# Performance work log

Measured on AMD Instinct MI355X. Metric: run time of the kernel, lower is better.

## Reference

```python
import jax, jax.numpy as jnp
import numpy as np

B, IN, D1, H1, H2, NC = 16384, 1024, 8, 2048, 1024, 1000
C = IN // D1  # 128 channels, D=8 each
EPS = 1e-5


def _bn(x, g, b):
    # training-mode BatchNorm1d: biased variance over batch dim
    m = jnp.mean(x, axis=0)
    v = jnp.var(x, axis=0)
    return (x - m) * jax.lax.rsqrt(v + EPS) * g + b


def setup_inputs() -> dict:
    key = jax.random.key(0)
    ks = jax.random.split(key, 18)
    f = jax.random.normal
    return {
        "x": f(ks[0], (B, IN), jnp.float32),
        "norm0_g": 1.0 + 0.1 * f(ks[1], (IN,), jnp.float32),
        "norm0_b": 0.1 * f(ks[2], (IN,), jnp.float32),
        "S": f(ks[3], (C, D1, 15), jnp.float32),
        "Hm": f(ks[4], (15, 16), jnp.float32),
        "T": f(ks[5], (C, 15), jnp.float32),
        "LUT": f(ks[6], (C, 16, D1), jnp.float32),
        "W1": 0.02 * f(ks[7], (H1, IN), jnp.float32),
        "b1": 0.02 * f(ks[8], (H1,), jnp.float32),
        "norm1_g": 1.0 + 0.1 * f(ks[9], (H1,), jnp.float32),
        "norm1_b": 0.1 * f(ks[10], (H1,), jnp.float32),
        "W2": 0.02 * f(ks[11], (H2, H1), jnp.float32),
        "b2": 0.02 * f(ks[12], (H2,), jnp.float32),
        "norm2_g": 1.0 + 0.1 * f(ks[13], (H2,), jnp.float32),
        "norm2_b": 0.1 * f(ks[14], (H2,), jnp.float32),
        "W3": 0.02 * f(ks[15], (NC, H2), jnp.float32),
        "b3": 0.02 * f(ks[16], (NC,), jnp.float32),
    }


def reference(x, norm0_g, norm0_b, S, Hm, T, LUT, W1, b1,
              norm1_g, norm1_b, W2, b2, norm2_g, norm2_b, W3, b3):
    h = _bn(x, norm0_g, norm0_b)
    # --- MM block: per-channel small GEMMs + STE sign + STE argmax LUT ---
    xc = h.reshape(-1, C, D1)                          # [B, C, D]
    z = jnp.einsum('bcd,cdk->bck', xc, S) - T - 1e-4   # [B, C, 15]
    t = jnp.tanh(z)
    q = jax.lax.stop_gradient(jnp.sign(z) - t) + t     # STE sign
    logits = jnp.einsum('bck,kj->bcj', q, Hm)          # [B, C, 16]
    one_hot = jax.nn.one_hot(jnp.argmax(logits, axis=-1), 16, dtype=logits.dtype)
    sm = jax.nn.softmax(logits, axis=-1)
    oh_out = jnp.einsum('bck,ckd->bcd', one_hot, LUT)
    sm_out = jnp.einsum('bck,ckd->bcd', sm, LUT)
    v = jax.lax.stop_gradient(oh_out - sm_out) + sm_out  # STE argmax select
    v = v.reshape(-1, C * D1)                           # [B, IN]
    # --- MLP head ---
    h1 = jax.nn.relu(_bn(v @ W1.T + b1, norm1_g, norm1_b))
    h2 = jax.nn.relu(_bn(h1 @ W2.T + b2, norm2_g, norm2_b))
    logits3 = h2 @ W3.T + b3
    return jax.nn.log_softmax(logits3, axis=-1), h1
```

## Files before the change

kernel.cpp:

```cpp
#include <hip/hip_runtime.h>

typedef unsigned short u16;
typedef __attribute__((ext_vector_type(8))) short bf16x8;
typedef __attribute__((ext_vector_type(4))) float f32x4;
typedef __attribute__((ext_vector_type(4))) u16 u16x4;
typedef __attribute__((ext_vector_type(8))) u16 u16x8;

__device__ __forceinline__ u16 f2bf(float f) {
    union { float f; unsigned u; } v; v.f = f;
    unsigned u = v.u;
    unsigned r = (u + 0x7fffu + ((u >> 16) & 1u)) >> 16;
    return (u16)r;
}
__device__ __forceinline__ float bf2f(u16 u) {
    union { unsigned u; float f; } v; v.u = ((unsigned)u) << 16;
    return v.f;
}

__device__ __forceinline__ void gload16(const u16* g, u16* l) {
    __builtin_amdgcn_global_load_lds((const __attribute__((address_space(1))) void*)g,
                                     (__attribute__((address_space(3))) void*)l, 16, 0, 0);
}

#define WAITV(N) asm volatile("s_waitcnt vmcnt(" #N ")" ::: "memory")

__device__ __forceinline__ void sbar() {
    __builtin_amdgcn_sched_barrier(0);
    __builtin_amdgcn_s_barrier();
    __builtin_amdgcn_sched_barrier(0);
}

__device__ __forceinline__ void cvt4(const float* in, u16* out, int i) {
    f32x4 v = *(const f32x4*)(in + (size_t)i * 4);
    u16x4 o;
    o.x = f2bf(v.x); o.y = f2bf(v.y); o.z = f2bf(v.z); o.w = f2bf(v.w);
    *(u16x4*)(out + (size_t)i * 4) = o;
}

__global__ __launch_bounds__(256) void leaf_kernel(
    const float* __restrict__ W1, const float* __restrict__ W2, const float* __restrict__ W3,
    u16* __restrict__ W1b, u16* __restrict__ W2b, u16* __restrict__ W3b,
    const float* __restrict__ x, float* __restrict__ part0) {
    int bid = blockIdx.x;
    if (bid < 5120) {
        int i = bid * 256 + threadIdx.x;
        if (i < 524288) {
            cvt4(W1, W1b, i);
        } else if (i < 1048576) {
            cvt4(W2, W2b, i - 524288);
        } else {
            int j = i - 1048576;
            int e = j * 4;
            int row = e >> 10;
            u16x4 o;
            if (row < 1000) {
                f32x4 v = *(const f32x4*)(W3 + e);
                o.x = f2bf(v.x); o.y = f2bf(v.y); o.z = f2bf(v.z); o.w = f2bf(v.w);
            } else {
                o.x = 0; o.y = 0; o.z = 0; o.w = 0;
            }
            *(u16x4*)(W3b + e) = o;
        }
    } else {
        int by = bid - 5120;
        int col = threadIdx.x * 4;
        long base = (long)by * 32 * 1024 + col;
        f32x4 s = {0.f, 0.f, 0.f, 0.f};
        f32x4 q = {0.f, 0.f, 0.f, 0.f};
        for (int r = 0; r < 32; ++r) {
            f32x4 v = *(const f32x4*)(x + base + (long)r * 1024);
            s.x += v.x; s.y += v.y; s.z += v.z; s.w += v.w;
            q.x = fmaf(v.x, v.x, q.x); q.y = fmaf(v.y, v.y, q.y);
            q.z = fmaf(v.z, v.z, q.z); q.w = fmaf(v.w, v.w, q.w);
        }
        long o = ((long)by * 1024 + col) * 2;
        f32x4 p0 = {s.x, q.x, s.y, q.y};
        f32x4 p1 = {s.z, q.z, s.w, q.w};
        *(f32x4*)(part0 + o) = p0;
        *(f32x4*)(part0 + o + 4) = p1;
    }
}

__global__ __launch_bounds__(256) void col_stats_finalize(
    const float* __restrict__ part, int cols, int nblk, float inv_n,
    const float* __restrict__ g, const float* __restrict__ b, float* __restrict__ ab) {
    __shared__ float red[8][64];
    int cl = threadIdx.x & 31;
    int j = threadIdx.x >> 5;
    int col = blockIdx.x * 32 + cl;
    int per = nblk / 8;
    float s = 0.f, ss = 0.f;
    for (int i = 0; i < per; ++i) {
        long o = ((long)(j * per + i) * cols + col) * 2;
        s += part[o]; ss += part[o + 1];
    }
    red[j][cl * 2] = s;
    red[j][cl * 2 + 1] = ss;
    __syncthreads();
    if (threadIdx.x < 32) {
        int c = blockIdx.x * 32 + threadIdx.x;
        float fs = 0.f, fss = 0.f;
#pragma unroll
        for (int jj = 0; jj < 8; ++jj) {
            fs += red[jj][threadIdx.x * 2];
            fss += red[jj][threadIdx.x * 2 + 1];
        }
        float m = fs * inv_n;
        float var = fss * inv_n - m * m;
        float a = g[c] * rsqrtf(var + 1e-5f);
        ab[c * 2 + 0] = a;
        ab[c * 2 + 1] = b[c] - m * a;
    }
}

__global__ __launch_bounds__(256) void mm_block_kernel(
    const float* __restrict__ x, const float* __restrict__ ab0,
    const float* __restrict__ S, const float* __restrict__ Tt,
    const float* __restrict__ Hm, const float* __restrict__ LUT,
    u16* __restrict__ v) {
    __shared__ float sS[480];
    __shared__ float sT[60];
    __shared__ float sHm[240];
    __shared__ float sLUT[512];
    __shared__ float sAB[64];
    const int t = threadIdx.x;
    const int cb = blockIdx.y * 4;

    for (int i = t; i < 480; i += 256) sS[i] = S[cb * 120 + i];
    for (int i = t; i < 60; i += 256)  sT[i] = Tt[cb * 15 + i];
    for (int i = t; i < 240; i += 256) sHm[i] = Hm[i];
    for (int i = t; i < 512; i += 256) sLUT[i] = LUT[cb * 128 + i];
    for (int i = t; i < 64; i += 256)  sAB[i] = ab0[cb * 16 + i];
    __syncthreads();

    const int row = blockIdx.x * 256 + t;
    const float* xp = x + (size_t)row * 1024 + cb * 8;
    float xr[32];
#pragma unroll
    for (int i = 0; i < 8; ++i) {
        f32x4 v4 = *(const f32x4*)(xp + i * 4);
        xr[i * 4 + 0] = v4.x; xr[i * 4 + 1] = v4.y;
        xr[i * 4 + 2] = v4.z; xr[i * 4 + 3] = v4.w;
    }
    u16 ov[32];
#pragma unroll
    for (int ch = 0; ch < 4; ++ch) {
        float h[8];
#pragma unroll
        for (int d = 0; d < 8; ++d)
            h[d] = xr[ch * 8 + d] * sAB[ch * 16 + d * 2] + sAB[ch * 16 + d * 2 + 1];
        float lg[16];
#pragma unroll
        for (int j = 0; j < 16; ++j) lg[j] = 0.f;
        for (int k = 0; k < 15; ++k) {
            float a = 0.f;
#pragma unroll
            for (int d = 0; d < 8; ++d) a = fmaf(h[d], sS[ch * 120 + d * 15 + k], a);
            float z = (a - sT[ch * 15 + k]) - 1e-4f;
            float q = (z > 0.f) ? 1.f : ((z < 0.f) ? -1.f : 0.f);
#pragma unroll
            for (int j = 0; j < 16; ++j) lg[j] = fmaf(q, sHm[k * 16 + j], lg[j]);
        }
        int jb = 0; float best = lg[0];
#pragma unroll
        for (int j = 1; j < 16; ++j) { if (lg[j] > best) { best = lg[j]; jb = j; } }
#pragma unroll
        for (int d = 0; d < 8; ++d) ov[ch * 8 + d] = f2bf(sLUT[ch * 128 + jb * 8 + d]);
    }
    u16* vp = v + (size_t)row * 1024 + cb * 8;
#pragma unroll
    for (int ch = 0; ch < 4; ++ch)
        *(u16x8*)(vp + ch * 8) = *(u16x8*)&ov[ch * 8];
}

__global__ __launch_bounds__(256) void bn_relu_apply8(
    const u16* __restrict__ y, const float* __restrict__ ab, int cols, int total8,
    float* __restrict__ out_f32, u16* __restrict__ out_b16) {
    int i = blockIdx.x * 256 + threadIdx.x;
    if (i >= total8) return;
    long e = (long)i * 8;
    int col = (int)(e % cols);
    u16x8 yv = *(const u16x8*)(y + e);
    float r[8];
#pragma unroll
    for (int d = 0; d < 8; ++d)
        r[d] = fmaxf(bf2f(yv[d]) * ab[(col + d) * 2] + ab[(col + d) * 2 + 1], 0.f);
    if (out_f32) {
        f32x4 rf0 = {r[0], r[1], r[2], r[3]};
        f32x4 rf1 = {r[4], r[5], r[6], r[7]};
        *(f32x4*)(out_f32 + e) = rf0;
        *(f32x4*)(out_f32 + e + 4) = rf1;
    }
    u16x8 o;
#pragma unroll
    for (int d = 0; d < 8; ++d) o[d] = f2bf(r[d]);
    *(u16x8*)(out_b16 + e) = o;
}

#define MFMA16(a, b, c) __builtin_amdgcn_mfma_f32_16x16x32_bf16(a, b, c, 0, 0, 0)

template <bool STORE_BF16, bool DO_STATS, bool WRITER>
__global__ __launch_bounds__(512, 2) void gemm256(
    const u16* __restrict__ A, const u16* __restrict__ Bm, void* __restrict__ Cv,
    const float* __restrict__ bias, float* __restrict__ part,
    int M, int N, int K, int ldc, int ncol,
    const u16* __restrict__ wsrc, float* __restrict__ wdst, long wn4) {
    extern __shared__ u16 lds[];
    const int t = threadIdx.x;
    const int gyG = WRITER ? ((int)gridDim.y - 2) : (int)gridDim.y;
    if (WRITER && (int)blockIdx.y >= gyG) {
        long wblk = (long)((int)blockIdx.y - gyG) * gridDim.x + blockIdx.x;
        long tid = wblk * 512 + t;
        for (long c = tid; c < wn4; c += 65536) {
            u16x4 v = *(const u16x4*)(wsrc + c * 4);
            f32x4 o = {bf2f(v.x), bf2f(v.y), bf2f(v.z), bf2f(v.w)};
            __builtin_nontemporal_store(o, (f32x4*)(wdst + c * 4));
        }
        return;
    }
    const int BOFF = 32768;
    const int lane = t & 63, w = t >> 6;
    const int wr = w >> 2, wc = w & 3;
    const int fr = lane & 15, kg = lane >> 4;
    const int gx = gridDim.x;
    const int nwg = gx * gyG;
    const int flat = blockIdx.y * gx + blockIdx.x;
    const int swz = (flat & 7) * (nwg >> 3) + (flat >> 3);
    const int bm = (swz % gx) * 256;
    const int bn = (swz / gx) * 256;
    const int NT = K >> 6;

    const int srow8 = lane >> 3;
    const int scc = (lane & 7) ^ srow8;
    const int L0 = w * 2;
    const u16* gAb = A + ((size_t)bm + L0 * 8 + srow8) * K + scc * 8;
    const u16* gBb = Bm + ((size_t)bn + L0 * 8 + srow8) * K + scc * 8;
    u16* ldsW = lds + L0 * 512 + lane * 8;

    const int s0 = (kg ^ (fr & 7)) * 8;
    const int s1 = s0 ^ 32;
    int rA[4], rB[2];
#pragma unroll
    for (int i = 0; i < 4; ++i) rA[i] = (i * 32 + wr * 16 + fr) * 64;
#pragma unroll
    for (int p = 0; p < 2; ++p) rB[p] = (p * 64 + wc * 16 + fr) * 64;

    f32x4 acc[8][4];
#pragma unroll
    for (int m = 0; m < 8; ++m)
#pragma unroll
        for (int n = 0; n < 4; ++n) acc[m][n] = (f32x4){0.f, 0.f, 0.f, 0.f};

    bf16x8 Ar[8][2], Br[2][2];

#define STG(gp, matOff, d, half, k0)                                          \
    {                                                                         \
        u16* dst_ = ldsW + (matOff) + ((d) * 2 + (half)) * 8192;              \
        const u16* src_ = (gp) + (size_t)((half) * 128) * K + (k0);           \
        gload16(src_, dst_);                                                  \
        gload16(src_ + (size_t)8 * K, dst_ + 512);                            \
    }
#define LDF(off) (*(const bf16x8*)&lds[off])

    STG(gAb, 0, 0, 0, 0);
    STG(gBb, BOFF, 0, 0, 0);
    STG(gAb, 0, 0, 1, 0);
    STG(gBb, BOFF, 0, 1, 0);

#pragma unroll 2
    for (int tt = 0; tt < NT - 1; ++tt) {
        const int d = tt & 1, dn = d ^ 1;
        const int k0n = (tt + 1) << 6;
        const int a0 = (d * 2) * 8192, a1 = (d * 2 + 1) * 8192;
        const int b0 = BOFF + a0, b1 = BOFF + a1;
        WAITV(4); sbar();
        STG(gAb, 0, dn, 0, k0n);
#pragma unroll
        for (int i = 0; i < 4; ++i) { Ar[i][0] = LDF(a0 + rA[i] + s0); Ar[i][1] = LDF(a0 + rA[i] + s1); }
#pragma unroll
        for (int p = 0; p < 2; ++p) { Br[p][0] = LDF(b0 + rB[p] + s0); Br[p][1] = LDF(b0 + rB[p] + s1); }
        __builtin_amdgcn_s_setprio(1);
#pragma unroll
        for (int i = 0; i < 4; ++i)
#pragma unroll
            for (int p = 0; p < 2; ++p) {
                acc[i][p] = MFMA16(Ar[i][0], Br[p][0], acc[i][p]);
                acc[i][p] = MFMA16(Ar[i][1], Br[p][1], acc[i][p]);
            }
        __builtin_amdgcn_s_setprio(0);
        WAITV(4); sbar();
        STG(gBb, BOFF, dn, 0, k0n);
#pragma unroll
        for (int i = 0; i < 4; ++i) { Ar[4 + i][0] = LDF(a1 + rA[i] + s0); Ar[4 + i][1] = LDF(a1 + rA[i] + s1); }
        __builtin_amdgcn_s_setprio(1);
#pragma unroll
        for (int i = 0; i < 4; ++i)
#pragma unroll
            for (int p = 0; p < 2; ++p) {
                acc[4 + i][p] = MFMA16(Ar[4 + i][0], Br[p][0], acc[4 + i][p]);
                acc[4 + i][p] = MFMA16(Ar[4 + i][1], Br[p][1], acc[4 + i][p]);
            }
        __builtin_amdgcn_s_setprio(0);
        WAITV(4); sbar();
        STG(gAb, 0, dn, 1, k0n);
#pragma unroll
        for (int p = 0; p < 2; ++p) { Br[p][0] = LDF(b1 + rB[p] + s0); Br[p][1] = LDF(b1 + rB[p] + s1); }
        __builtin_amdgcn_s_setprio(1);
#pragma unroll
        for (int i = 0; i < 4; ++i)
#pragma unroll
            for (int p = 0; p < 2; ++p) {
                acc[4 + i][2 + p] = MFMA16(Ar[4 + i][0], Br[p][0], acc[4 + i][2 + p]);
                acc[4 + i][2 + p] = MFMA16(Ar[4 + i][1], Br[p][1], acc[4 + i][2 + p]);
            }
        __builtin_amdgcn_s_setprio(0);
        STG(gBb, BOFF, dn, 1, k0n);
        __builtin_amdgcn_s_setprio(1);
#pragma unroll
        for (int i = 0; i < 4; ++i)
#pragma unroll
            for (int p = 0; p < 2; ++p) {
                acc[i][2 + p] = MFMA16(Ar[i][0], Br[p][0], acc[i][2 + p]);
                acc[i][2 + p] = MFMA16(Ar[i][1], Br[p][1], acc[i][2 + p]);
            }
        __builtin_amdgcn_s_setprio(0);
    }
    {
        const int d = (NT - 1) & 1;
        const int a0 = (d * 2) * 8192, a1 = (d * 2 + 1) * 8192;
        const int b0 = BOFF + a0, b1 = BOFF + a1;
        WAITV(4); sbar();
#pragma unroll
        for (int i = 0; i < 4; ++i) { Ar[i][0] = LDF(a0 + rA[i] + s0); Ar[i][1] = LDF(a0 + rA[i] + s1); }
#pragma unroll
        for (int p = 0; p < 2; ++p) { Br[p][0] = LDF(b0 + rB[p] + s0); Br[p][1] = LDF(b0 + rB[p] + s1); }
        __builtin_amdgcn_s_setprio(1);
#pragma unroll
        for (int i = 0; i < 4; ++i)
#pragma unroll
            for (int p = 0; p < 2; ++p) {
                acc[i][p] = MFMA16(Ar[i][0], Br[p][0], acc[i][p]);
                acc[i][p] = MFMA16(Ar[i][1], Br[p][1], acc[i][p]);
            }
        __builtin_amdgcn_s_setprio(0);
        WAITV(2); sbar();
#pragma unroll
        for (int i = 0; i < 4; ++i) { Ar[4 + i][0] = LDF(a1 + rA[i] + s0); Ar[4 + i][1] = LDF(a1 + rA[i] + s1); }
        __builtin_amdgcn_s_setprio(1);
#pragma unroll
        for (int i = 0; i < 4; ++i)
#pragma unroll
            for (int p = 0; p < 2; ++p) {
                acc[4 + i][p] = MFMA16(Ar[4 + i][0], Br[p][0], acc[4 + i][p]);
                acc[4 + i][p] = MFMA16(Ar[4 + i][1], Br[p][1], acc[4 + i][p]);
            }
        __builtin_amdgcn_s_setprio(0);
        WAITV(0); sbar();
#pragma unroll
        for (int p = 0; p < 2; ++p) { Br[p][0] = LDF(b1 + rB[p] + s0); Br[p][1] = LDF(b1 + rB[p] + s1); }
        __builtin_amdgcn_s_setprio(1);
#pragma unroll
        for (int i = 0; i < 4; ++i)
#pragma unroll
            for (int p = 0; p < 2; ++p) {
                acc[4 + i][2 + p] = MFMA16(Ar[4 + i][0], Br[p][0], acc[4 + i][2 + p]);
                acc[4 + i][2 + p] = MFMA16(Ar[4 + i][1], Br[p][1], acc[4 + i][2 + p]);
                acc[i][2 + p] = MFMA16(Ar[i][0], Br[p][0], acc[i][2 + p]);
                acc[i][2 + p] = MFMA16(Ar[i][1], Br[p][1], acc[i][2 + p]);
            }
        __builtin_amdgcn_s_setprio(0);
    }

    const int fq = lane >> 4;
    if (STORE_BF16) {
        u16* C = (u16*)Cv;
        u16* sm = lds;
        const int orow = t >> 4;
        const int ocol = (t & 15) * 16;
#pragma unroll
        for (int m = 0; m < 8; ++m) {
            __syncthreads();
#pragma unroll
            for (int n = 0; n < 4; ++n)
#pragma unroll
                for (int j = 0; j < 4; ++j)
                    sm[(wr * 16 + fq * 4 + j) * 256 + n * 64 + wc * 16 + fr] = f2bf(acc[m][n][j]);
            __syncthreads();
            u16x8 o0 = *(const u16x8*)&sm[orow * 256 + ocol];
            u16x8 o1 = *(const u16x8*)&sm[orow * 256 + ocol + 8];
            u16* cp = C + (size_t)(bm + m * 32 + orow) * ldc + bn + ocol;
            *(u16x8*)cp = o0;
            *(u16x8*)(cp + 8) = o1;
        }
    } else {
#pragma unroll
        for (int m = 0; m < 8; ++m) {
#pragma unroll
            for (int n = 0; n < 4; ++n) {
                int row = bm + m * 32 + wr * 16 + fq * 4;
                int col = bn + n * 64 + wc * 16 + fr;
                if (col < ncol) {
                    float* C = (float*)Cv;
                    float bv = bias ? bias[col] : 0.f;
#pragma unroll
                    for (int j = 0; j < 4; ++j)
                        C[(size_t)(row + j) * ldc + col] = acc[m][n][j] + bv;
                }
            }
        }
    }

    if (DO_STATS) {
        __syncthreads();
        float* smf = (float*)lds;
        float sv[4], qv[4];
#pragma unroll
        for (int n = 0; n < 4; ++n) {
            float s = 0.f, q = 0.f;
#pragma unroll
            for (int m = 0; m < 8; ++m)
#pragma unroll
                for (int j = 0; j < 4; ++j) {
                    float vv = acc[m][n][j];
                    s += vv;
                    q = fmaf(vv, vv, q);
                }
            s += __shfl_xor(s, 16); s += __shfl_xor(s, 32);
            q += __shfl_xor(q, 16); q += __shfl_xor(q, 32);
            sv[n] = s; qv[n] = q;
        }
        if (lane < 16) {
#pragma unroll
            for (int n = 0; n < 4; ++n) {
                smf[(w * 64 + n * 16 + lane) * 2 + 0] = sv[n];
                smf[(w * 64 + n * 16 + lane) * 2 + 1] = qv[n];
            }
        }
        __syncthreads();
        if (t < 256) {
            int n = t >> 6, wcq = (t >> 4) & 3, frq = t & 15;
            int i0 = (wcq * 64 + n * 16 + frq) * 2;
            int i1 = ((4 + wcq) * 64 + n * 16 + frq) * 2;
            long o = ((long)(bm >> 8) * N + bn + t) * 2;
            part[o] = smf[i0] + smf[i1];
            part[o + 1] = smf[i0 + 1] + smf[i1 + 1];
        }
    }
#undef STG
#undef LDF
}

__global__ __launch_bounds__(256) void log_softmax_wave(float* __restrict__ y) {
    const int w = threadIdx.x >> 6;
    const int lane = threadIdx.x & 63;
    float* p = y + ((size_t)blockIdx.x * 4 + w) * 1000;
    const bool has3 = lane < 58;
    f32x4 v0 = ((const f32x4*)p)[lane];
    f32x4 v1 = ((const f32x4*)p)[lane + 64];
    f32x4 v2 = ((const f32x4*)p)[lane + 128];
    f32x4 v3 = has3 ? ((const f32x4*)p)[lane + 192]
                    : (f32x4){-1e30f, -1e30f, -1e30f, -1e30f};
    float m = fmaxf(fmaxf(fmaxf(v0.x, v0.y), fmaxf(v0.z, v0.w)),
                    fmaxf(fmaxf(v1.x, v1.y), fmaxf(v1.z, v1.w)));
    m = fmaxf(m, fmaxf(fmaxf(v2.x, v2.y), fmaxf(v2.z, v2.w)));
    m = fmaxf(m, fmaxf(fmaxf(v3.x, v3.y), fmaxf(v3.z, v3.w)));
#pragma unroll
    for (int d = 32; d > 0; d >>= 1) m = fmaxf(m, __shfl_xor(m, d));
    float sum = expf(v0.x - m) + expf(v0.y - m) + expf(v0.z - m) + expf(v0.w - m)
              + expf(v1.x - m) + expf(v1.y - m) + expf(v1.z - m) + expf(v1.w - m)
              + expf(v2.x - m) + expf(v2.y - m) + expf(v2.z - m) + expf(v2.w - m)
              + expf(v3.x - m) + expf(v3.y - m) + expf(v3.z - m) + expf(v3.w - m);
#pragma unroll
    for (int d = 32; d > 0; d >>= 1) sum += __shfl_xor(sum, d);
    float lse = m + logf(sum);
    v0.x -= lse; v0.y -= lse; v0.z -= lse; v0.w -= lse;
    v1.x -= lse; v1.y -= lse; v1.z -= lse; v1.w -= lse;
    v2.x -= lse; v2.y -= lse; v2.z -= lse; v2.w -= lse;
    __builtin_nontemporal_store(v0, &((f32x4*)p)[lane]);
    __builtin_nontemporal_store(v1, &((f32x4*)p)[lane + 64]);
    __builtin_nontemporal_store(v2, &((f32x4*)p)[lane + 128]);
    if (has3) {
        v3.x -= lse; v3.y -= lse; v3.z -= lse; v3.w -= lse;
        __builtin_nontemporal_store(v3, &((f32x4*)p)[lane + 192]);
    }
}

extern "C" void kernel_launch(void* const* d_in, const int* in_sizes, int n_in,
                              void* d_out, int out_size, void* d_ws, size_t ws_size,
                              hipStream_t stream) {
    const float* x   = (const float*)d_in[0];
    const float* n0g = (const float*)d_in[1];
    const float* n0b = (const float*)d_in[2];
    const float* S   = (const float*)d_in[3];
    const float* Hm  = (const float*)d_in[4];
    const float* Tt  = (const float*)d_in[5];
    const float* LUT = (const float*)d_in[6];
    const float* W1  = (const float*)d_in[7];
    const float* n1g = (const float*)d_in[9];
    const float* n1b = (const float*)d_in[10];
    const float* W2  = (const float*)d_in[11];
    const float* n2g = (const float*)d_in[13];
    const float* n2b = (const float*)d_in[14];
    const float* W3  = (const float*)d_in[15];
    const float* b3  = (const float*)d_in[16];

    const int B = 16384, IN = 1024, H1 = 2048, H2 = 1024;
    const int NBY0 = 512;

    hipFuncSetAttribute((const void*)&gemm256<true, true, false>,
                        hipFuncAttributeMaxDynamicSharedMemorySize, 131072);
    hipFuncSetAttribute((const void*)&gemm256<true, true, true>,
                        hipFuncAttributeMaxDynamicSharedMemorySize, 131072);
    hipFuncSetAttribute((const void*)&gemm256<false, false, false>,
                        hipFuncAttributeMaxDynamicSharedMemorySize, 131072);

    char* ws = (char*)d_ws;
    size_t off = 0;
    auto alloc = [&](size_t bytes) -> char* {
        char* p = ws + off;
        off += (bytes + 255) & ~(size_t)255;
        return p;
    };
    float* ab0  = (float*)alloc(IN * 2 * sizeof(float));
    float* ab1  = (float*)alloc(H1 * 2 * sizeof(float));
    float* ab2  = (float*)alloc(H2 * 2 * sizeof(float));
    float* part0 = (float*)alloc((size_t)NBY0 * IN * 2 * sizeof(float));
    float* part1 = (float*)alloc((size_t)(B / 256) * H1 * 2 * sizeof(float));
    float* part2 = (float*)alloc((size_t)(B / 256) * H2 * 2 * sizeof(float));
    u16* W1b = (u16*)alloc((size_t)H1 * IN * 2);
    u16* W2b = (u16*)alloc((size_t)H2 * H1 * 2);
    u16* W3b = (u16*)alloc((size_t)1024 * 1024 * 2);
    u16* vb  = (u16*)alloc((size_t)B * IN * 2);
    u16* y1b = (u16*)alloc((size_t)B * H1 * 2);

    float* out0 = (float*)d_out;
    float* out1 = out0 + (size_t)B * 1000;

    leaf_kernel<<<5120 + NBY0, 256, 0, stream>>>(W1, W2, W3, W1b, W2b, W3b, x, part0);

    col_stats_finalize<<<IN / 32, 256, 0, stream>>>(part0, IN, NBY0, 1.f / B, n0g, n0b, ab0);

    mm_block_kernel<<<dim3(B / 256, 32), 256, 0, stream>>>(x, ab0, S, Tt, Hm, LUT, vb);

    gemm256<true, true, false><<<dim3(B / 256, H1 / 256), 512, 131072, stream>>>(
        vb, W1b, y1b, nullptr, part1, B, H1, IN, H1, H1, nullptr, nullptr, 0);

    col_stats_finalize<<<H1 / 32, 256, 0, stream>>>(part1, H1, B / 256, 1.f / B, n1g, n1b, ab1);
    bn_relu_apply8<<<B * H1 / 8 / 256, 256, 0, stream>>>(y1b, ab1, H1, B * H1 / 8, nullptr, y1b);

    gemm256<true, true, true><<<dim3(B / 256, H2 / 256 + 2), 512, 131072, stream>>>(
        y1b, W2b, vb, nullptr, part2, B, H2, H1, H2, H2,
        y1b, out1, (long)B * H1 / 4);

    col_stats_finalize<<<H2 / 32, 256, 0, stream>>>(part2, H2, B / 256, 1.f / B, n2g, n2b, ab2);
    bn_relu_apply8<<<B * H2 / 8 / 256, 256, 0, stream>>>(vb, ab2, H2, B * H2 / 8, nullptr, vb);

    gemm256<false, false, false><<<dim3(B / 256, 1024 / 256), 512, 131072, stream>>>(
        vb, W3b, out0, b3, nullptr, B, 1024, H2, 1000, 1000, nullptr, nullptr, 0);

    log_softmax_wave<<<B / 4, 256, 0, stream>>>(out0);
}
```

Before: 357.8 us.

## Fuse log-softmax into final GEMM epilogue via grid-wide atomic barrier

Removes the separate log_softmax kernel. The last GEMM now adds the bias and computes per-tile row max and sum-exp, then writes those partials to a workspace. An atomic-counter spin barrier across all workgroups follows, after which each block combines the four column-tile partials into a row log-sum-exp and stores the normalized logits directly. This avoids re-reading and re-writing the 16384x1000 fp32 output. In exchange it relies on all 256 workgroups being co-resident and on `nwg` being defined, otherwise the spin barrier can deadlock.

```diff
diff --git a/kernel.cpp b/kernel.cpp
--- a/kernel.cpp
+++ b/kernel.cpp
@@ -40,8 +40,9 @@
 __global__ __launch_bounds__(256) void leaf_kernel(
     const float* __restrict__ W1, const float* __restrict__ W2, const float* __restrict__ W3,
     u16* __restrict__ W1b, u16* __restrict__ W2b, u16* __restrict__ W3b,
-    const float* __restrict__ x, float* __restrict__ part0) {
+    const float* __restrict__ x, float* __restrict__ part0, int* __restrict__ cnt) {
     int bid = blockIdx.x;
+    if (bid == 0 && threadIdx.x == 0) *cnt = 0;
     if (bid < 5120) {
         int i = bid * 256 + threadIdx.x;
         if (i < 524288) {
@@ -199,12 +200,13 @@
 
 #define MFMA16(a, b, c) __builtin_amdgcn_mfma_f32_16x16x32_bf16(a, b, c, 0, 0, 0)
 
-template <bool STORE_BF16, bool DO_STATS, bool WRITER>
+template <bool STORE_BF16, bool DO_STATS, bool WRITER, bool SMAX>
 __global__ __launch_bounds__(512, 2) void gemm256(
     const u16* __restrict__ A, const u16* __restrict__ Bm, void* __restrict__ Cv,
     const float* __restrict__ bias, float* __restrict__ part,
     int M, int N, int K, int ldc, int ncol,
-    const u16* __restrict__ wsrc, float* __restrict__ wdst, long wn4) {
+    const u16* __restrict__ wsrc, float* __restrict__ wdst, long wn4,
+    int* __restrict__ cnt) {
     extern __shared__ u16 lds[];
     const int t = threadIdx.x;
     const int gyG = WRITER ? ((int)gridDim.y - 2) : (int)gridDim.y;
@@ -392,6 +394,94 @@
             *(u16x8*)cp = o0;
             *(u16x8*)(cp + 8) = o1;
         }
+    } else if (SMAX) {
+        float* out = (float*)Cv;
+        float* smf = (float*)lds;
+        float bv[4]; bool vld[4]; int cc[4];
+#pragma unroll
+        for (int n = 0; n < 4; ++n) {
+            cc[n] = bn + n * 64 + wc * 16 + fr;
+            vld[n] = cc[n] < ncol;
+            bv[n] = vld[n] ? bias[cc[n]] : 0.f;
+        }
+#pragma unroll
+        for (int m = 0; m < 8; ++m)
+#pragma unroll
+            for (int n = 0; n < 4; ++n)
+#pragma unroll
+                for (int j = 0; j < 4; ++j) acc[m][n][j] += bv[n];
+        __syncthreads();
+#pragma unroll
+        for (int m = 0; m < 8; ++m) {
+#pragma unroll
+            for (int j = 0; j < 4; ++j) {
+                float mx = -1e30f;
+#pragma unroll
+                for (int n = 0; n < 4; ++n) if (vld[n]) mx = fmaxf(mx, acc[m][n][j]);
+                mx = fmaxf(mx, __shfl_xor(mx, 1));
+                mx = fmaxf(mx, __shfl_xor(mx, 2));
+                mx = fmaxf(mx, __shfl_xor(mx, 4));
+                mx = fmaxf(mx, __shfl_xor(mx, 8));
+                float se = 0.f;
+#pragma unroll
+                for (int n = 0; n < 4; ++n) if (vld[n]) se += expf(acc[m][n][j] - mx);
+                se += __shfl_xor(se, 1);
+                se += __shfl_xor(se, 2);
+                se += __shfl_xor(se, 4);
+                se += __shfl_xor(se, 8);
+                if (fr == 0) {
+                    int rl = m * 32 + wr * 16 + kg * 4 + j;
+                    smf[(wc * 256 + rl) * 2] = mx;
+                    smf[(wc * 256 + rl) * 2 + 1] = se;
+                }
+            }
+        }
+        __syncthreads();
+        if (t < 256) {
+            float m0 = smf[(0 * 256 + t) * 2], sA = smf[(0 * 256 + t) * 2 + 1];
+            float m1 = smf[(1 * 256 + t) * 2], sB = smf[(1 * 256 + t) * 2 + 1];
+            float m2 = smf[(2 * 256 + t) * 2], sC = smf[(2 * 256 + t) * 2 + 1];
+            float m3 = smf[(3 * 256 + t) * 2], sD = smf[(3 * 256 + t) * 2 + 1];
+            float Mm = fmaxf(fmaxf(m0, m1), fmaxf(m2, m3));
+            float Ss = sA * expf(m0 - Mm) + sB * expf(m1 - Mm)
+                     + sC * expf(m2 - Mm) + sD * expf(m3 - Mm);
+            long o = ((long)(bn >> 8) * M + bm + t) * 2;
+            part[o] = Mm;
+            part[o + 1] = Ss;
+        }
+        __syncthreads();
+        if (t == 0) {
+            __threadfence();
+            atomicAdd(cnt, 1);
+            while (atomicAdd(cnt, 0) < nwg) {}
+            __threadfence();
+        }
+        __syncthreads();
+        if (t < 256) {
+            int row = bm + t;
+            float m0 = part[((long)0 * M + row) * 2], sA = part[((long)0 * M + row) * 2 + 1];
+            float m1 = part[((long)1 * M + row) * 2], sB = part[((long)1 * M + row) * 2 + 1];
+            float m2 = part[((long)2 * M + row) * 2], sC = part[((long)2 * M + row) * 2 + 1];
+            float m3 = part[((long)3 * M + row) * 2], sD = part[((long)3 * M + row) * 2 + 1];
+            float Mm = fmaxf(fmaxf(m0, m1), fmaxf(m2, m3));
+            float Ss = sA * expf(m0 - Mm) + sB * expf(m1 - Mm)
+                     + sC * expf(m2 - Mm) + sD * expf(m3 - Mm);
+            smf[t] = Mm + logf(Ss);
+        }
+        __syncthreads();
+#pragma unroll
+        for (int m = 0; m < 8; ++m) {
+#pragma unroll
+            for (int j = 0; j < 4; ++j) {
+                int rl = m * 32 + wr * 16 + fq * 4 + j;
+                float lse = smf[rl];
+#pragma unroll
+                for (int n = 0; n < 4; ++n)
+                    if (vld[n])
+                        __builtin_nontemporal_store(acc[m][n][j] - lse,
+                            &out[(size_t)(bm + rl) * ldc + cc[n]]);
+            }
+        }
     } else {
 #pragma unroll
         for (int m = 0; m < 8; ++m) {
@@ -401,10 +491,10 @@
                 int col = bn + n * 64 + wc * 16 + fr;
                 if (col < ncol) {
                     float* C = (float*)Cv;
-                    float bv = bias ? bias[col] : 0.f;
+                    float bvv = bias ? bias[col] : 0.f;
 #pragma unroll
                     for (int j = 0; j < 4; ++j)
-                        C[(size_t)(row + j) * ldc + col] = acc[m][n][j] + bv;
+                        C[(size_t)(row + j) * ldc + col] = acc[m][n][j] + bvv;
                 }
             }
         }
@@ -448,41 +538,6 @@
     }
 #undef STG
 #undef LDF
-}
-
-__global__ __launch_bounds__(256) void log_softmax_wave(float* __restrict__ y) {
-    const int w = threadIdx.x >> 6;
-    const int lane = threadIdx.x & 63;
-    float* p = y + ((size_t)blockIdx.x * 4 + w) * 1000;
-    const bool has3 = lane < 58;
-    f32x4 v0 = ((const f32x4*)p)[lane];
-    f32x4 v1 = ((const f32x4*)p)[lane + 64];
-    f32x4 v2 = ((const f32x4*)p)[lane + 128];
-    f32x4 v3 = has3 ? ((const f32x4*)p)[lane + 192]
-                    : (f32x4){-1e30f, -1e30f, -1e30f, -1e30f};
-    float m = fmaxf(fmaxf(fmaxf(v0.x, v0.y), fmaxf(v0.z, v0.w)),
-                    fmaxf(fmaxf(v1.x, v1.y), fmaxf(v1.z, v1.w)));
-    m = fmaxf(m, fmaxf(fmaxf(v2.x, v2.y), fmaxf(v2.z, v2.w)));
-    m = fmaxf(m, fmaxf(fmaxf(v3.x, v3.y), fmaxf(v3.z, v3.w)));
-#pragma unroll
-    for (int d = 32; d > 0; d >>= 1) m = fmaxf(m, __shfl_xor(m, d));
-    float sum = expf(v0.x - m) + expf(v0.y - m) + expf(v0.z - m) + expf(v0.w - m)
-              + expf(v1.x - m) + expf(v1.y - m) + expf(v1.z - m) + expf(v1.w - m)
-              + expf(v2.x - m) + expf(v2.y - m) + expf(v2.z - m) + expf(v2.w - m)
-              + expf(v3.x - m) + expf(v3.y - m) + expf(v3.z - m) + expf(v3.w - m);
-#pragma unroll
-    for (int d = 32; d > 0; d >>= 1) sum += __shfl_xor(sum, d);
-    float lse = m + logf(sum);
-    v0.x -= lse; v0.y -= lse; v0.z -= lse; v0.w -= lse;
-    v1.x -= lse; v1.y -= lse; v1.z -= lse; v1.w -= lse;
-    v2.x -= lse; v2.y -= lse; v2.z -= lse; v2.w -= lse;
-    __builtin_nontemporal_store(v0, &((f32x4*)p)[lane]);
-    __builtin_nontemporal_store(v1, &((f32x4*)p)[lane + 64]);
-    __builtin_nontemporal_store(v2, &((f32x4*)p)[lane + 128]);
-    if (has3) {
-        v3.x -= lse; v3.y -= lse; v3.z -= lse; v3.w -= lse;
-        __builtin_nontemporal_store(v3, &((f32x4*)p)[lane + 192]);
-    }
 }
 
 extern "C" void kernel_launch(void* const* d_in, const int* in_sizes, int n_in,
@@ -507,11 +562,11 @@
     const int B = 16384, IN = 1024, H1 = 2048, H2 = 1024;
     const int NBY0 = 512;
 
-    hipFuncSetAttribute((const void*)&gemm256<true, true, false>,
+    hipFuncSetAttribute((const void*)&gemm256<true, true, false, false>,
                         hipFuncAttributeMaxDynamicSharedMemorySize, 131072);
-    hipFuncSetAttribute((const void*)&gemm256<true, true, true>,
+    hipFuncSetAttribute((const void*)&gemm256<true, true, true, false>,
                         hipFuncAttributeMaxDynamicSharedMemorySize, 131072);
-    hipFuncSetAttribute((const void*)&gemm256<false, false, false>,
+    hipFuncSetAttribute((const void*)&gemm256<false, false, false, true>,
                         hipFuncAttributeMaxDynamicSharedMemorySize, 131072);
 
     char* ws = (char*)d_ws;
@@ -521,12 +576,14 @@
         off += (bytes + 255) & ~(size_t)255;
         return p;
     };
+    int*   cnt  = (int*)alloc(256);
     float* ab0  = (float*)alloc(IN * 2 * sizeof(float));
     float* ab1  = (float*)alloc(H1 * 2 * sizeof(float));
     float* ab2  = (float*)alloc(H2 * 2 * sizeof(float));
     float* part0 = (float*)alloc((size_t)NBY0 * IN * 2 * sizeof(float));
     float* part1 = (float*)alloc((size_t)(B / 256) * H1 * 2 * sizeof(float));
     float* part2 = (float*)alloc((size_t)(B / 256) * H2 * 2 * sizeof(float));
+    float* part3 = (float*)alloc((size_t)4 * B * 2 * sizeof(float));
     u16* W1b = (u16*)alloc((size_t)H1 * IN * 2);
     u16* W2b = (u16*)alloc((size_t)H2 * H1 * 2);
     u16* W3b = (u16*)alloc((size_t)1024 * 1024 * 2);
@@ -536,27 +593,25 @@
     float* out0 = (float*)d_out;
     float* out1 = out0 + (size_t)B * 1000;
 
-    leaf_kernel<<<5120 + NBY0, 256, 0, stream>>>(W1, W2, W3, W1b, W2b, W3b, x, part0);
+    leaf_kernel<<<5120 + NBY0, 256, 0, stream>>>(W1, W2, W3, W1b, W2b, W3b, x, part0, cnt);
 
     col_stats_finalize<<<IN / 32, 256, 0, stream>>>(part0, IN, NBY0, 1.f / B, n0g, n0b, ab0);
 
     mm_block_kernel<<<dim3(B / 256, 32), 256, 0, stream>>>(x, ab0, S, Tt, Hm, LUT, vb);
 
-    gemm256<true, true, false><<<dim3(B / 256, H1 / 256), 512, 131072, stream>>>(
-        vb, W1b, y1b, nullptr, part1, B, H1, IN, H1, H1, nullptr, nullptr, 0);
+    gemm256<true, true, false, false><<<dim3(B / 256, H1 / 256), 512, 131072, stream>>>(
+        vb, W1b, y1b, nullptr, part1, B, H1, IN, H1, H1, nullptr, nullptr, 0, nullptr);
 
     col_stats_finalize<<<H1 / 32, 256, 0, stream>>>(part1, H1, B / 256, 1.f / B, n1g, n1b, ab1);
     bn_relu_apply8<<<B * H1 / 8 / 256, 256, 0, stream>>>(y1b, ab1, H1, B * H1 / 8, nullptr, y1b);
 
-    gemm256<true, true, true><<<dim3(B / 256, H2 / 256 + 2), 512, 131072, stream>>>(
+    gemm256<true, true, true, false><<<dim3(B / 256, H2 / 256 + 2), 512, 131072, stream>>>(
         y1b, W2b, vb, nullptr, part2, B, H2, H1, H2, H2,
-        y1b, out1, (long)B * H1 / 4);
+        y1b, out1, (long)B * H1 / 4, nullptr);
 
     col_stats_finalize<<<H2 / 32, 256, 0, stream>>>(part2, H2, B / 256, 1.f / B, n2g, n2b, ab2);
     bn_relu_apply8<<<B * H2 / 8 / 256, 256, 0, stream>>>(vb, ab2, H2, B * H2 / 8, nullptr, vb);
 
-    gemm256<false, false, false><<<dim3(B / 256, 1024 / 256), 512, 131072, stream>>>(
-        vb, W3b, out0, b3, nullptr, B, 1024, H2, 1000, 1000, nullptr, nullptr, 0);
-
-    log_softmax_wave<<<B / 4, 256, 0, stream>>>(out0);
-}
+    gemm256<false, false, false, true><<<dim3(B / 256, 1024 / 256), 512, 131072, stream>>>(
+        vb, W3b, out0, b3, part3, B, 1024, H2, 1000, 1000, nullptr, nullptr, 0, cnt);
+}
```

Measured after the change: 389.4 us. +8.8%, slower.
